# Optimization experiments

Measured on AMD Instinct MI355X. Metric: run time of the kernel, lower is better.

## Reference

```python
import jax, jax.numpy as jnp
import numpy as np

R, H, E = 200000, 256, 100000  # num_relations, hidden_dim, num_hyperedges


def setup_inputs() -> dict:
    key = jax.random.key(0)
    ks = jax.random.split(key, 8)
    rng = np.random.default_rng(0)
    # ragged hyperedge sizes in [1, 15], avg ~8 -> total ~800k src entries
    sizes = rng.integers(1, 16, size=E)
    total = int(sizes.sum())
    he_ptr = jnp.asarray(np.concatenate([[0], np.cumsum(sizes)]), dtype=jnp.int64)
    he_src = jax.random.randint(ks[0], (total,), 0, R, dtype=jnp.int64)
    # unique targets make the scatter deterministic and equivalent)
    he_tgt = jnp.asarray(rng.permutation(R)[:E], dtype=jnp.int64)
    he_w = jax.random.uniform(ks[1], (E,), dtype=jnp.float32)
    x = jax.random.normal(ks[2], (R, H), dtype=jnp.float32)
    s = 1.0 / np.sqrt(H)
    W_msg = jax.random.uniform(ks[3], (H, H), jnp.float32, -s, s)
    b_msg = jnp.zeros((H,), jnp.float32)
    W_gate = jax.random.uniform(ks[4], (2 * H, H), jnp.float32, -s, s)
    b_gate = jnp.zeros((H,), jnp.float32)
    W_upd = jax.random.uniform(ks[5], (H, H), jnp.float32, -s, s)
    b_upd = jnp.zeros((H,), jnp.float32)
    return {"x": x, "he_ptr": he_ptr, "he_src": he_src, "he_tgt": he_tgt,
            "he_w": he_w, "W_msg": W_msg, "b_msg": b_msg,
            "W_gate": W_gate, "b_gate": b_gate, "W_upd": W_upd, "b_upd": b_upd}


def reference(x, he_ptr, he_src, he_tgt, he_w, W_msg, b_msg, W_gate, b_gate, W_upd, b_upd):
    total = he_src.shape[0]
    num_e = he_tgt.shape[0]
    # segment id of each src entry: which hyperedge it belongs to
    seg = jnp.searchsorted(he_ptr, jnp.arange(total), side="right") - 1
    gathered = x[he_src]                                   # [total, H]
    sums = jax.ops.segment_sum(gathered, seg, num_segments=num_e)  # [E, H]
    counts = (he_ptr[1:] - he_ptr[:-1]).astype(x.dtype)    # [E]
    src_mean = sums / counts[:, None]                      # segment mean
    msg = src_mean @ W_msg + b_msg                         # [E, H]
    tgt_x = x[he_tgt]                                      # [E, H]
    gate = jax.nn.sigmoid(jnp.concatenate([tgt_x, msg], axis=-1) @ W_gate + b_gate)
    upd = tgt_x + he_w[:, None] * gate * msg               # gated residual
    out = x.at[he_tgt].set(upd)                            # unique targets
    out = jnp.clip(out @ W_upd + b_upd, 0.0, 1.0)          # clipped relu
    return out
```

## Files before the change

### kernel.cpp

```cpp
#include <hip/hip_runtime.h>
#include <math.h>

#define H 256

typedef __attribute__((ext_vector_type(8))) short short8;
typedef __attribute__((ext_vector_type(4))) float f32x4;
typedef __attribute__((ext_vector_type(4))) int int4v;
typedef __attribute__((ext_vector_type(2))) unsigned int uint2v;
typedef unsigned short ushort_t;

__device__ __forceinline__ float bf2f(unsigned short u) {
    union { unsigned int i; float f; } v; v.i = ((unsigned int)u) << 16; return v.f;
}
__device__ __forceinline__ unsigned short f2bf(float f) {
    union { float f; unsigned int i; } v; v.f = f;
    unsigned int r = v.i + 0x7FFFu + ((v.i >> 16) & 1u);
    return (unsigned short)(r >> 16);
}
__device__ __forceinline__ void glds16(const void* g, void* l) {
    __builtin_amdgcn_global_load_lds((const __attribute__((address_space(1))) void*)g,
                                     (__attribute__((address_space(3))) void*)l, 16, 0, 0);
}
__device__ __forceinline__ int4v pack_f32x8_bf16(const float* p) {
    float4 f0 = *(const float4*)(p);
    float4 f1 = *(const float4*)(p + 4);
    int4v d;
    d.x = (int)((unsigned)f2bf(f0.x) | ((unsigned)f2bf(f0.y) << 16));
    d.y = (int)((unsigned)f2bf(f0.z) | ((unsigned)f2bf(f0.w) << 16));
    d.z = (int)((unsigned)f2bf(f1.x) | ((unsigned)f2bf(f1.y) << 16));
    d.w = (int)((unsigned)f2bf(f1.z) | ((unsigned)f2bf(f1.w) << 16));
    return d;
}

__global__ void prep_weights(const float* __restrict__ Wm, const float* __restrict__ Wg,
                             const float* __restrict__ Wu,
                             ushort_t* __restrict__ Wmt, ushort_t* __restrict__ Wgt,
                             ushort_t* __restrict__ Wut) {
    int idx = blockIdx.x * 256 + threadIdx.x;
    if (idx < 65536) {
        int n = idx >> 8, k = idx & 255;
        Wmt[idx] = f2bf(Wm[(size_t)k * 256 + n]);
        Wut[idx] = f2bf(Wu[(size_t)k * 256 + n]);
    }
    if (idx < 131072) {
        int n = idx >> 9, k = idx & 511;
        Wgt[idx] = f2bf(Wg[(size_t)k * 256 + n]);
    }
}

__global__ void imap_init(int* __restrict__ imap, int R) {
    int r = blockIdx.x * 256 + threadIdx.x;
    if (r < R) imap[r] = -1;
}
__global__ void imap_scatter(const int* __restrict__ tgt, int* __restrict__ imap, int E) {
    int e = blockIdx.x * 256 + threadIdx.x;
    if (e < E) imap[tgt[e]] = e;
}

__global__ void conv_bf16(const float* __restrict__ x, ushort_t* __restrict__ yb, size_t n8) {
    size_t i = (size_t)blockIdx.x * blockDim.x + threadIdx.x;
    size_t stride = (size_t)gridDim.x * blockDim.x;
    for (; i < n8; i += stride)
        *(int4v*)(yb + i * 8) = pack_f32x8_bf16(x + i * 8);
}

__global__ __launch_bounds__(256) void seg_mean_bf16(const ushort_t* __restrict__ yb,
                                                     const int* __restrict__ ptr,
                                                     const int* __restrict__ src,
                                                     ushort_t* __restrict__ smb, int E) {
    int e = blockIdx.x * 4 + (threadIdx.x >> 6);
    if (e >= E) return;
    int lane = threadIdx.x & 63;
    int s = ptr[e], t = ptr[e + 1];
    float a0 = 0.f, a1 = 0.f, a2 = 0.f, a3 = 0.f;
    int i = s;
    for (; i + 4 <= t; i += 4) {
        uint2v v0 = *(const uint2v*)(yb + (size_t)src[i + 0] * H + lane * 4);
        uint2v v1 = *(const uint2v*)(yb + (size_t)src[i + 1] * H + lane * 4);
        uint2v v2 = *(const uint2v*)(yb + (size_t)src[i + 2] * H + lane * 4);
        uint2v v3 = *(const uint2v*)(yb + (size_t)src[i + 3] * H + lane * 4);
        a0 += bf2f(v0.x & 0xffff) + bf2f(v1.x & 0xffff) + bf2f(v2.x & 0xffff) + bf2f(v3.x & 0xffff);
        a1 += bf2f(v0.x >> 16)    + bf2f(v1.x >> 16)    + bf2f(v2.x >> 16)    + bf2f(v3.x >> 16);
        a2 += bf2f(v0.y & 0xffff) + bf2f(v1.y & 0xffff) + bf2f(v2.y & 0xffff) + bf2f(v3.y & 0xffff);
        a3 += bf2f(v0.y >> 16)    + bf2f(v1.y >> 16)    + bf2f(v2.y >> 16)    + bf2f(v3.y >> 16);
    }
    for (; i < t; ++i) {
        uint2v v = *(const uint2v*)(yb + (size_t)src[i] * H + lane * 4);
        a0 += bf2f(v.x & 0xffff); a1 += bf2f(v.x >> 16);
        a2 += bf2f(v.y & 0xffff); a3 += bf2f(v.y >> 16);
    }
    float inv = 1.f / (float)(t - s);
    uint2v o;
    o.x = (unsigned)f2bf(a0 * inv) | ((unsigned)f2bf(a1 * inv) << 16);
    o.y = (unsigned)f2bf(a2 * inv) | ((unsigned)f2bf(a3 * inv) << 16);
    *(uint2v*)(smb + (size_t)e * H + lane * 4) = o;
}

__global__ __launch_bounds__(256) void seg_mean_f32w(const float* __restrict__ x,
                                                     const int* __restrict__ ptr,
                                                     const int* __restrict__ src,
                                                     ushort_t* __restrict__ smb, int E) {
    int e = blockIdx.x * 4 + (threadIdx.x >> 6);
    if (e >= E) return;
    int lane = threadIdx.x & 63;
    int s = ptr[e], t = ptr[e + 1];
    float a0 = 0.f, a1 = 0.f, a2 = 0.f, a3 = 0.f;
    int i = s;
    for (; i + 4 <= t; i += 4) {
        float4 v0 = *(const float4*)(x + (size_t)src[i + 0] * H + lane * 4);
        float4 v1 = *(const float4*)(x + (size_t)src[i + 1] * H + lane * 4);
        float4 v2 = *(const float4*)(x + (size_t)src[i + 2] * H + lane * 4);
        float4 v3 = *(const float4*)(x + (size_t)src[i + 3] * H + lane * 4);
        a0 += v0.x + v1.x + v2.x + v3.x;
        a1 += v0.y + v1.y + v2.y + v3.y;
        a2 += v0.z + v1.z + v2.z + v3.z;
        a3 += v0.w + v1.w + v2.w + v3.w;
    }
    for (; i < t; ++i) {
        float4 v = *(const float4*)(x + (size_t)src[i] * H + lane * 4);
        a0 += v.x; a1 += v.y; a2 += v.z; a3 += v.w;
    }
    float inv = 1.f / (float)(t - s);
    uint2v o;
    o.x = (unsigned)f2bf(a0 * inv) | ((unsigned)f2bf(a1 * inv) << 16);
    o.y = (unsigned)f2bf(a2 * inv) | ((unsigned)f2bf(a3 * inv) << 16);
    *(uint2v*)(smb + (size_t)e * H + lane * 4) = o;
}

template<int MODE, int KTOT, bool XB>
__global__ __launch_bounds__(256) void mfma_gemm(
    const ushort_t* __restrict__ Abf,
    const float* __restrict__ Xf,
    const ushort_t* __restrict__ Xb,
    const ushort_t* __restrict__ Aux,
    const int* __restrict__ Idx,
    const float* __restrict__ Hew,
    const ushort_t* __restrict__ Wt,
    const float* __restrict__ Bias,
    ushort_t* __restrict__ OutB,
    float* __restrict__ OutF,
    int M)
{
    constexpr int NT = KTOT / 32;
    const int m0 = blockIdx.x * 128;
    const int c0 = blockIdx.y * 128;
    const int tid = threadIdx.x;
    const int wv = tid >> 6;
    const int lane = tid & 63;
    const int wr = wv >> 1, wc = wv & 1;

    __shared__ __align__(16) ushort_t As[2][128 * 32];
    __shared__ __align__(16) ushort_t Bs[2][128 * 32];

    f32x4 acc[4][4];
#pragma unroll
    for (int i = 0; i < 4; ++i)
#pragma unroll
        for (int j = 0; j < 4; ++j) acc[i][j] = (f32x4){0.f, 0.f, 0.f, 0.f};

    const int ch0 = wv * 64 + lane;
    const int ch1 = ch0 + 256;

    auto stageB = [&](int buf, int k0) {
#pragma unroll
        for (int c = 0; c < 2; ++c) {
            int ch = c ? ch1 : ch0;
            int col = ch >> 2, sl = ch & 3, cc = sl ^ ((col >> 1) & 3);
            glds16(Wt + (size_t)(c0 + col) * KTOT + (k0 + cc * 8),
                   (char*)(&Bs[buf][0]) + ch * 16);
        }
    };

    auto stageA = [&](int buf, int k0) {
#pragma unroll
        for (int c = 0; c < 2; ++c) {
            int ch = c ? ch1 : ch0;
            int row = ch >> 2, sl = ch & 3, cc = sl ^ ((row >> 1) & 3);
            int kg = k0 + cc * 8;
            int r = m0 + row; if (r > M - 1) r = M - 1;
            if constexpr (MODE == 0) {
                glds16(Abf + (size_t)r * KTOT + kg, (char*)(&As[buf][0]) + ch * 16);
            } else {
                int4v d;
                if constexpr (MODE == 1) {
                    if (k0 < 256) {
                        int tr = Idx[r];
                        if constexpr (XB) d = *(const int4v*)(Xb + (size_t)tr * 256 + kg);
                        else              d = pack_f32x8_bf16(Xf + (size_t)tr * 256 + kg);
                    } else {
                        d = *(const int4v*)(Aux + (size_t)r * 256 + (kg - 256));
                    }
                } else {
                    int e = Idx[r];
                    if (e >= 0) d = *(const int4v*)(Aux + (size_t)e * 256 + kg);
                    else if constexpr (XB) d = *(const int4v*)(Xb + (size_t)r * 256 + kg);
                    else d = pack_f32x8_bf16(Xf + (size_t)r * 256 + kg);
                }
                *(int4v*)((char*)(&As[buf][0]) + ch * 16) = d;
            }
        }
    };

    auto compute = [&](int buf) {
        short8 a[4], b[4];
#pragma unroll
        for (int fm = 0; fm < 4; ++fm) {
            int row = wr * 64 + fm * 16 + (lane & 15);
            int byte = (row * 4 + ((lane >> 4) ^ ((row >> 1) & 3))) * 16;
            a[fm] = *(const short8*)((const char*)(&As[buf][0]) + byte);
        }
#pragma unroll
        for (int fn = 0; fn < 4; ++fn) {
            int col = wc * 64 + fn * 16 + (lane & 15);
            int byte = (col * 4 + ((lane >> 4) ^ ((col >> 1) & 3))) * 16;
            b[fn] = *(const short8*)((const char*)(&Bs[buf][0]) + byte);
        }
#pragma unroll
        for (int fm = 0; fm < 4; ++fm)
#pragma unroll
            for (int fn = 0; fn < 4; ++fn)
                acc[fm][fn] = __builtin_amdgcn_mfma_f32_16x16x32_bf16(a[fm], b[fn], acc[fm][fn], 0, 0, 0);
    };

    stageA(0, 0); stageB(0, 0);
    __syncthreads();
    for (int kt = 0; kt < NT; ++kt) {
        if (kt + 1 < NT) { stageA((kt + 1) & 1, (kt + 1) * 32); stageB((kt + 1) & 1, (kt + 1) * 32); }
        compute(kt & 1);
        __syncthreads();
    }

#pragma unroll
    for (int fm = 0; fm < 4; ++fm) {
        int rbase = m0 + wr * 64 + fm * 16 + (lane >> 4) * 4;
#pragma unroll
        for (int fn = 0; fn < 4; ++fn) {
            int col = c0 + wc * 64 + fn * 16 + (lane & 15);
            float bia = Bias[col];
            f32x4 v = acc[fm][fn];
#pragma unroll
            for (int i = 0; i < 4; ++i) {
                int rg = rbase + i;
                if (rg < M) {
                    float z = v[i] + bia;
                    if constexpr (MODE == 0) {
                        OutB[(size_t)rg * 256 + col] = f2bf(z);
                    } else if constexpr (MODE == 1) {
                        float g = 1.f / (1.f + __expf(-z));
                        int tr = Idx[rg];
                        float tx;
                        if constexpr (XB) tx = bf2f(Xb[(size_t)tr * 256 + col]);
                        else              tx = Xf[(size_t)tr * 256 + col];
                        float m = bf2f(Aux[(size_t)rg * 256 + col]);
                        float u = tx + Hew[rg] * g * m;
                        OutB[(size_t)rg * 256 + col] = f2bf(u);
                    } else {
                        OutF[(size_t)rg * 256 + col] = fminf(fmaxf(z, 0.f), 1.f);
                    }
                }
            }
        }
    }
}

extern "C" void kernel_launch(void* const* d_in, const int* in_sizes, int n_in,
                              void* d_out, int out_size, void* d_ws, size_t ws_size,
                              hipStream_t stream) {
    const float* x      = (const float*)d_in[0];
    const int*   he_ptr = (const int*)d_in[1];
    const int*   he_src = (const int*)d_in[2];
    const int*   he_tgt = (const int*)d_in[3];
    const float* he_w   = (const float*)d_in[4];
    const float* W_msg  = (const float*)d_in[5];
    const float* b_msg  = (const float*)d_in[6];
    const float* W_gate = (const float*)d_in[7];
    const float* b_gate = (const float*)d_in[8];
    const float* W_upd  = (const float*)d_in[9];
    const float* b_upd  = (const float*)d_in[10];

    const int E = in_sizes[3];
    const int R = in_sizes[0] / H;

    const size_t wbytes = (size_t)(65536 + 131072 + 65536) * 2;
    const size_t needA = (size_t)R * H * 2 + (size_t)E * H * 2 * 2 + (size_t)R * 4 + wbytes;
    const bool bigws = ws_size >= needA;

    dim3 gE((E + 127) / 128, 2);
    dim3 gR((R + 127) / 128, 2);

    if (bigws) {
        char* ws = (char*)d_ws;
        ushort_t* yb   = (ushort_t*)ws;
        ushort_t* buf0 = yb + (size_t)R * H;
        ushort_t* buf1 = buf0 + (size_t)E * H;
        int*      imap = (int*)(buf1 + (size_t)E * H);
        ushort_t* Wmt  = (ushort_t*)((char*)imap + (size_t)R * 4);
        ushort_t* Wgt  = Wmt + 256 * 256;
        ushort_t* Wut  = Wgt + 256 * 512;

        prep_weights<<<512, 256, 0, stream>>>(W_msg, W_gate, W_upd, Wmt, Wgt, Wut);
        imap_init<<<(R + 255) / 256, 256, 0, stream>>>(imap, R);
        imap_scatter<<<(E + 255) / 256, 256, 0, stream>>>(he_tgt, imap, E);
        conv_bf16<<<2048, 256, 0, stream>>>(x, yb, (size_t)R * H / 8);
        seg_mean_bf16<<<(E + 3) / 4, 256, 0, stream>>>(yb, he_ptr, he_src, buf0, E);

        mfma_gemm<0, 256, true><<<gE, 256, 0, stream>>>(buf0, nullptr, yb, nullptr, nullptr, nullptr,
                                                        Wmt, b_msg, buf1, nullptr, E);
        mfma_gemm<1, 512, true><<<gE, 256, 0, stream>>>(nullptr, nullptr, yb, buf1, he_tgt, he_w,
                                                        Wgt, b_gate, buf0, nullptr, E);
        mfma_gemm<2, 256, true><<<gR, 256, 0, stream>>>(nullptr, nullptr, yb, buf0, imap, nullptr,
                                                        Wut, b_upd, nullptr, (float*)d_out, R);
    } else {
        char* ws = (char*)d_ws;
        ushort_t* buf0 = (ushort_t*)ws;
        ushort_t* buf1 = buf0 + (size_t)E * H;
        int*      imap = (int*)(buf1 + (size_t)E * H);
        ushort_t* Wmt  = (ushort_t*)((char*)imap + (size_t)R * 4);
        ushort_t* Wgt  = Wmt + 256 * 256;
        ushort_t* Wut  = Wgt + 256 * 512;

        prep_weights<<<512, 256, 0, stream>>>(W_msg, W_gate, W_upd, Wmt, Wgt, Wut);
        imap_init<<<(R + 255) / 256, 256, 0, stream>>>(imap, R);
        imap_scatter<<<(E + 255) / 256, 256, 0, stream>>>(he_tgt, imap, E);
        seg_mean_f32w<<<(E + 3) / 4, 256, 0, stream>>>(x, he_ptr, he_src, buf0, E);

        mfma_gemm<0, 256, false><<<gE, 256, 0, stream>>>(buf0, nullptr, nullptr, nullptr, nullptr, nullptr,
                                                         Wmt, b_msg, buf1, nullptr, E);
        mfma_gemm<1, 512, false><<<gE, 256, 0, stream>>>(nullptr, x, nullptr, buf1, he_tgt, he_w,
                                                         Wgt, b_gate, buf0, nullptr, E);
        mfma_gemm<2, 256, false><<<gR, 256, 0, stream>>>(nullptr, x, nullptr, buf0, imap, nullptr,
                                                         Wut, b_upd, nullptr, (float*)d_out, R);
    }
}
```

Measured before the change: 418.5 us.

## Widen GEMM blocks to full 256-column output with 512 threads

Result: faster. 372.8 us (-10.9%).

```diff
diff --git a/kernel.cpp b/kernel.cpp
--- a/kernel.cpp
+++ b/kernel.cpp
@@ -127,8 +127,24 @@
     *(uint2v*)(smb + (size_t)e * H + lane * 4) = o;
 }
 
+#define LOADA_CHUNK(k0v, d)                                                              \
+    do {                                                                                 \
+        if constexpr (MODE == 1) {                                                       \
+            if ((k0v) < 256) {                                                           \
+                if constexpr (XB) d = *(const int4v*)(pX + (k0v));                       \
+                else              d = pack_f32x8_bf16(pXf + (k0v));                      \
+            } else {                                                                     \
+                d = *(const int4v*)(pA + ((k0v) - 256));                                 \
+            }                                                                            \
+        } else {                                                                         \
+            if constexpr (XB) d = *(const int4v*)(p2 + (k0v));                           \
+            else { if (!useF) d = *(const int4v*)(p2 + (k0v));                           \
+                   else       d = pack_f32x8_bf16(p2f + (k0v)); }                        \
+        }                                                                                \
+    } while (0)
+
 template<int MODE, int KTOT, bool XB>
-__global__ __launch_bounds__(256) void mfma_gemm(
+__global__ __launch_bounds__(512, 4) void wgemm(
     const ushort_t* __restrict__ Abf,
     const float* __restrict__ Xf,
     const ushort_t* __restrict__ Xb,
@@ -143,14 +159,48 @@
 {
     constexpr int NT = KTOT / 32;
     const int m0 = blockIdx.x * 128;
-    const int c0 = blockIdx.y * 128;
     const int tid = threadIdx.x;
     const int wv = tid >> 6;
     const int lane = tid & 63;
-    const int wr = wv >> 1, wc = wv & 1;
+    const int wr = wv >> 2, wc = wv & 3;
 
     __shared__ __align__(16) ushort_t As[2][128 * 32];
-    __shared__ __align__(16) ushort_t Bs[2][128 * 32];
+    __shared__ __align__(16) ushort_t Bs[2][256 * 32];
+
+    const int aRow  = tid >> 2;
+    const int sl    = tid & 3;
+    const int aCc   = sl ^ ((aRow >> 1) & 3);
+    const int bCol0 = tid >> 2;
+    const int bCol1 = bCol0 + 128;
+    const int bCc0  = sl ^ ((bCol0 >> 1) & 3);
+    const int bCc1  = sl ^ ((bCol1 >> 1) & 3);
+
+    const ushort_t* bSrc0 = Wt + (size_t)bCol0 * KTOT + bCc0 * 8;
+    const ushort_t* bSrc1 = Wt + (size_t)bCol1 * KTOT + bCc1 * 8;
+
+    int r = m0 + aRow; if (r > M - 1) r = M - 1;
+
+    const ushort_t* aSrc = nullptr;
+    const ushort_t* pX = nullptr;  const float* pXf = nullptr;
+    const ushort_t* pA = nullptr;
+    const ushort_t* p2 = nullptr;  const float* p2f = nullptr;
+    bool useF = false;
+    if constexpr (MODE == 0) {
+        aSrc = Abf + (size_t)r * KTOT + aCc * 8;
+    } else if constexpr (MODE == 1) {
+        int tr = Idx[r];
+        if constexpr (XB) pX = Xb + (size_t)tr * 256 + aCc * 8;
+        else              pXf = Xf + (size_t)tr * 256 + aCc * 8;
+        pA = Aux + (size_t)r * 256 + aCc * 8;
+    } else {
+        int e = Idx[r];
+        if constexpr (XB) {
+            p2 = (e >= 0 ? Aux + (size_t)e * 256 : Xb + (size_t)r * 256) + aCc * 8;
+        } else {
+            if (e >= 0) { p2 = Aux + (size_t)e * 256 + aCc * 8; useF = false; }
+            else        { p2f = Xf + (size_t)r * 256 + aCc * 8; useF = true; }
+        }
+    }
 
     f32x4 acc[4][4];
 #pragma unroll
@@ -158,84 +208,67 @@
 #pragma unroll
         for (int j = 0; j < 4; ++j) acc[i][j] = (f32x4){0.f, 0.f, 0.f, 0.f};
 
-    const int ch0 = wv * 64 + lane;
-    const int ch1 = ch0 + 256;
-
-    auto stageB = [&](int buf, int k0) {
-#pragma unroll
-        for (int c = 0; c < 2; ++c) {
-            int ch = c ? ch1 : ch0;
-            int col = ch >> 2, sl = ch & 3, cc = sl ^ ((col >> 1) & 3);
-            glds16(Wt + (size_t)(c0 + col) * KTOT + (k0 + cc * 8),
-                   (char*)(&Bs[buf][0]) + ch * 16);
-        }
-    };
-
-    auto stageA = [&](int buf, int k0) {
-#pragma unroll
-        for (int c = 0; c < 2; ++c) {
-            int ch = c ? ch1 : ch0;
-            int row = ch >> 2, sl = ch & 3, cc = sl ^ ((row >> 1) & 3);
-            int kg = k0 + cc * 8;
-            int r = m0 + row; if (r > M - 1) r = M - 1;
+    glds16(bSrc0, (char*)&Bs[0][0] + tid * 16);
+    glds16(bSrc1, (char*)&Bs[0][0] + (tid + 512) * 16);
+    if constexpr (MODE == 0) {
+        glds16(aSrc, (char*)&As[0][0] + tid * 16);
+    } else {
+        int4v d0; LOADA_CHUNK(0, d0);
+        *(int4v*)((char*)&As[0][0] + tid * 16) = d0;
+    }
+
+#pragma unroll 2
+    for (int kt = 0; kt < NT; ++kt) {
+        __syncthreads();
+        const int cur = kt & 1;
+        const int nxt = cur ^ 1;
+        const bool more = (kt + 1 < NT);
+        int4v pf;
+        if (more) {
+            const int k0 = (kt + 1) * 32;
+            glds16(bSrc0 + k0, (char*)&Bs[nxt][0] + tid * 16);
+            glds16(bSrc1 + k0, (char*)&Bs[nxt][0] + (tid + 512) * 16);
             if constexpr (MODE == 0) {
-                glds16(Abf + (size_t)r * KTOT + kg, (char*)(&As[buf][0]) + ch * 16);
+                glds16(aSrc + k0, (char*)&As[nxt][0] + tid * 16);
             } else {
-                int4v d;
-                if constexpr (MODE == 1) {
-                    if (k0 < 256) {
-                        int tr = Idx[r];
-                        if constexpr (XB) d = *(const int4v*)(Xb + (size_t)tr * 256 + kg);
-                        else              d = pack_f32x8_bf16(Xf + (size_t)tr * 256 + kg);
-                    } else {
-                        d = *(const int4v*)(Aux + (size_t)r * 256 + (kg - 256));
-                    }
-                } else {
-                    int e = Idx[r];
-                    if (e >= 0) d = *(const int4v*)(Aux + (size_t)e * 256 + kg);
-                    else if constexpr (XB) d = *(const int4v*)(Xb + (size_t)r * 256 + kg);
-                    else d = pack_f32x8_bf16(Xf + (size_t)r * 256 + kg);
-                }
-                *(int4v*)((char*)(&As[buf][0]) + ch * 16) = d;
+                LOADA_CHUNK(k0, pf);
             }
         }
-    };
-
-    auto compute = [&](int buf) {
-        short8 a[4], b[4];
-#pragma unroll
-        for (int fm = 0; fm < 4; ++fm) {
-            int row = wr * 64 + fm * 16 + (lane & 15);
-            int byte = (row * 4 + ((lane >> 4) ^ ((row >> 1) & 3))) * 16;
-            a[fm] = *(const short8*)((const char*)(&As[buf][0]) + byte);
-        }
+
+        const char* aBase = (const char*)&As[cur][0];
+        const char* bBase = (const char*)&Bs[cur][0];
+        const int kg = lane >> 4;
+        short8 a0, a1, a2, a3;
+        {
+            int r0 = wr * 64 + 0 * 16 + (lane & 15);
+            int r1 = r0 + 16, r2 = r0 + 32, r3 = r0 + 48;
+            a0 = *(const short8*)(aBase + (r0 * 4 + (kg ^ ((r0 >> 1) & 3))) * 16);
+            a1 = *(const short8*)(aBase + (r1 * 4 + (kg ^ ((r1 >> 1) & 3))) * 16);
+            a2 = *(const short8*)(aBase + (r2 * 4 + (kg ^ ((r2 >> 1) & 3))) * 16);
+            a3 = *(const short8*)(aBase + (r3 * 4 + (kg ^ ((r3 >> 1) & 3))) * 16);
+        }
+#pragma unroll
+        for (int fn = 0; fn < 4; ++fn) {
+            int cn = wc * 64 + fn * 16 + (lane & 15);
+            short8 b = *(const short8*)(bBase + (cn * 4 + (kg ^ ((cn >> 1) & 3))) * 16);
+            acc[0][fn] = __builtin_amdgcn_mfma_f32_16x16x32_bf16(a0, b, acc[0][fn], 0, 0, 0);
+            acc[1][fn] = __builtin_amdgcn_mfma_f32_16x16x32_bf16(a1, b, acc[1][fn], 0, 0, 0);
+            acc[2][fn] = __builtin_amdgcn_mfma_f32_16x16x32_bf16(a2, b, acc[2][fn], 0, 0, 0);
+            acc[3][fn] = __builtin_amdgcn_mfma_f32_16x16x32_bf16(a3, b, acc[3][fn], 0, 0, 0);
+        }
+        if (more) {
+            if constexpr (MODE != 0) {
+                *(int4v*)((char*)&As[nxt][0] + tid * 16) = pf;
+            }
+        }
+    }
+
+#pragma unroll
+    for (int fm = 0; fm < 4; ++fm) {
+        int rbase = m0 + wr * 64 + fm * 16 + (lane >> 4) * 4;
 #pragma unroll
         for (int fn = 0; fn < 4; ++fn) {
             int col = wc * 64 + fn * 16 + (lane & 15);
-            int byte = (col * 4 + ((lane >> 4) ^ ((col >> 1) & 3))) * 16;
-            b[fn] = *(const short8*)((const char*)(&Bs[buf][0]) + byte);
-        }
-#pragma unroll
-        for (int fm = 0; fm < 4; ++fm)
-#pragma unroll
-            for (int fn = 0; fn < 4; ++fn)
-                acc[fm][fn] = __builtin_amdgcn_mfma_f32_16x16x32_bf16(a[fm], b[fn], acc[fm][fn], 0, 0, 0);
-    };
-
-    stageA(0, 0); stageB(0, 0);
-    __syncthreads();
-    for (int kt = 0; kt < NT; ++kt) {
-        if (kt + 1 < NT) { stageA((kt + 1) & 1, (kt + 1) * 32); stageB((kt + 1) & 1, (kt + 1) * 32); }
-        compute(kt & 1);
-        __syncthreads();
-    }
-
-#pragma unroll
-    for (int fm = 0; fm < 4; ++fm) {
-        int rbase = m0 + wr * 64 + fm * 16 + (lane >> 4) * 4;
-#pragma unroll
-        for (int fn = 0; fn < 4; ++fn) {
-            int col = c0 + wc * 64 + fn * 16 + (lane & 15);
             float bia = Bias[col];
             f32x4 v = acc[fm][fn];
 #pragma unroll
@@ -285,8 +318,8 @@
     const size_t needA = (size_t)R * H * 2 + (size_t)E * H * 2 * 2 + (size_t)R * 4 + wbytes;
     const bool bigws = ws_size >= needA;
 
-    dim3 gE((E + 127) / 128, 2);
-    dim3 gR((R + 127) / 128, 2);
+    const int gE = (E + 127) / 128;
+    const int gR = (R + 127) / 128;
 
     if (bigws) {
         char* ws = (char*)d_ws;
@@ -304,12 +337,12 @@
         conv_bf16<<<2048, 256, 0, stream>>>(x, yb, (size_t)R * H / 8);
         seg_mean_bf16<<<(E + 3) / 4, 256, 0, stream>>>(yb, he_ptr, he_src, buf0, E);
 
-        mfma_gemm<0, 256, true><<<gE, 256, 0, stream>>>(buf0, nullptr, yb, nullptr, nullptr, nullptr,
-                                                        Wmt, b_msg, buf1, nullptr, E);
-        mfma_gemm<1, 512, true><<<gE, 256, 0, stream>>>(nullptr, nullptr, yb, buf1, he_tgt, he_w,
-                                                        Wgt, b_gate, buf0, nullptr, E);
-        mfma_gemm<2, 256, true><<<gR, 256, 0, stream>>>(nullptr, nullptr, yb, buf0, imap, nullptr,
-                                                        Wut, b_upd, nullptr, (float*)d_out, R);
+        wgemm<0, 256, true><<<gE, 512, 0, stream>>>(buf0, nullptr, yb, nullptr, nullptr, nullptr,
+                                                    Wmt, b_msg, buf1, nullptr, E);
+        wgemm<1, 512, true><<<gE, 512, 0, stream>>>(nullptr, nullptr, yb, buf1, he_tgt, he_w,
+                                                    Wgt, b_gate, buf0, nullptr, E);
+        wgemm<2, 256, true><<<gR, 512, 0, stream>>>(nullptr, nullptr, yb, buf0, imap, nullptr,
+                                                    Wut, b_upd, nullptr, (float*)d_out, R);
     } else {
         char* ws = (char*)d_ws;
         ushort_t* buf0 = (ushort_t*)ws;
@@ -324,11 +357,11 @@
         imap_scatter<<<(E + 255) / 256, 256, 0, stream>>>(he_tgt, imap, E);
         seg_mean_f32w<<<(E + 3) / 4, 256, 0, stream>>>(x, he_ptr, he_src, buf0, E);
 
-        mfma_gemm<0, 256, false><<<gE, 256, 0, stream>>>(buf0, nullptr, nullptr, nullptr, nullptr, nullptr,
-                                                         Wmt, b_msg, buf1, nullptr, E);
-        mfma_gemm<1, 512, false><<<gE, 256, 0, stream>>>(nullptr, x, nullptr, buf1, he_tgt, he_w,
-                                                         Wgt, b_gate, buf0, nullptr, E);
-        mfma_gemm<2, 256, false><<<gR, 256, 0, stream>>>(nullptr, x, nullptr, buf0, imap, nullptr,
-                                                         Wut, b_upd, nullptr, (float*)d_out, R);
-    }
-}
+        wgemm<0, 256, false><<<gE, 512, 0, stream>>>(buf0, nullptr, nullptr, nullptr, nullptr, nullptr,
+                                                     Wmt, b_msg, buf1, nullptr, E);
+        wgemm<1, 512, false><<<gE, 512, 0, stream>>>(nullptr, x, nullptr, buf1, he_tgt, he_w,
+                                                     Wgt, b_gate, buf0, nullptr, E);
+        wgemm<2, 256, false><<<gR, 512, 0, stream>>>(nullptr, x, nullptr, buf0, imap, nullptr,
+                                                     Wut, b_upd, nullptr, (float*)d_out, R);
+    }
+}
```
